# Kernel optimization log

Hardware: AMD Instinct MI355X
Metric: run time of the kernel (lower is better)

Reference implementation:

```python
import jax, jax.numpy as jnp
import numpy as np

S, B, D, H, F = 2048, 4, 1024, 16, 4096
DH = D // H  # per-head dim (nhid)
EPS = 1e-5


def layer_norm(x, g, b):
    m = jnp.mean(x, axis=-1, keepdims=True)
    v = jnp.mean((x - m) ** 2, axis=-1, keepdims=True)
    return (x - m) * jax.lax.rsqrt(v + EPS) * g + b


def setup_inputs() -> dict:
    key = jax.random.key(0)
    ks = jax.random.split(key, 16)
    s = 1.0 / np.sqrt(D)
    sf = 1.0 / np.sqrt(F)
    return {
        "x": jax.random.normal(ks[0], (S, B, D), dtype=jnp.float32),
        "ln1_g": jnp.ones((D,), jnp.float32),
        "ln1_b": jnp.zeros((D,), jnp.float32),
        "ln2_g": jnp.ones((D,), jnp.float32),
        "ln2_b": jnp.zeros((D,), jnp.float32),
        "Wq": jax.random.normal(ks[1], (D, D), jnp.float32) * s,
        "bq": jnp.zeros((D,), jnp.float32),
        "Wk": jax.random.normal(ks[2], (D, D), jnp.float32) * s,
        "bk": jnp.zeros((D,), jnp.float32),
        "Wv": jax.random.normal(ks[3], (D, D), jnp.float32) * s,
        "bv": jnp.zeros((D,), jnp.float32),
        "Wo": jax.random.normal(ks[4], (D, D), jnp.float32) * s,
        "bo": jnp.zeros((D,), jnp.float32),
        "W1": jax.random.normal(ks[5], (D, F), jnp.float32) * s,
        "b1": jnp.zeros((F,), jnp.float32),
        "W2": jax.random.normal(ks[6], (F, D), jnp.float32) * sf,
        "b2": jnp.zeros((D,), jnp.float32),
    }


def reference(x, ln1_g, ln1_b, ln2_g, ln2_b, Wq, bq, Wk, bk, Wv, bv, Wo, bo, W1, b1, W2, b2):
    # --- sublayer 0: LN -> full (non-causal) multi-head self-attention -> residual ---
    h = layer_norm(x, ln1_g, ln1_b)                      # [S,B,D]
    q = (h @ Wq + bq).reshape(S, B, H, DH)
    k = (h @ Wk + bk).reshape(S, B, H, DH)
    v = (h @ Wv + bv).reshape(S, B, H, DH)
    scale = 1.0 / jnp.sqrt(jnp.asarray(DH, x.dtype))
    scores = jnp.einsum("sbhd,tbhd->bhst", q, k) * scale  # [B,H,S,S]
    attn = jax.nn.softmax(scores, axis=-1)
    ctx = jnp.einsum("bhst,tbhd->sbhd", attn, v).reshape(S, B, D)
    x = x + (ctx @ Wo + bo)
    # --- sublayer 1: LN -> position-wise FFN -> residual ---
    h2 = layer_norm(x, ln2_g, ln2_b)
    ff = jax.nn.relu(h2 @ W1 + b1) @ W2 + b2
    return x + ff
```

## Files before the change

### kernel.cpp

```cpp
#include <hip/hip_runtime.h>
#include <hip/hip_bf16.h>
#include <stdint.h>

constexpr int S = 2048;
constexpr int B = 4;
constexpr int D = 1024;
constexpr int H = 16;
constexpr int F = 4096;
constexpr int DH = 64;
constexpr int N = S * B;

typedef __attribute__((ext_vector_type(8))) short  bf16x8;
typedef __attribute__((ext_vector_type(4))) float  floatx4;

__device__ __forceinline__ unsigned short f2bf(float f) {
    __hip_bfloat16 h = __float2bfloat16(f);
    return __builtin_bit_cast(unsigned short, h);
}
__device__ __forceinline__ uint32_t pack_bf2_fast(float a, float b) {
    uint32_t ua = __builtin_bit_cast(uint32_t, a) + 0x8000u;
    uint32_t ub = __builtin_bit_cast(uint32_t, b) + 0x8000u;
    return (ua >> 16) | (ub & 0xffff0000u);
}
__device__ __forceinline__ void glds16(const unsigned short* g, unsigned short* l) {
    __builtin_amdgcn_global_load_lds((__attribute__((address_space(1))) void*)(g),
                                     (__attribute__((address_space(3))) void*)(l),
                                     16, 0, 0);
}

__global__ __launch_bounds__(256) void convert_transpose(
    const float* __restrict__ src, unsigned short* __restrict__ dst, int K, int M) {
    __shared__ float tile[32][33];
    const int m0 = blockIdx.x * 32;
    const int k0 = blockIdx.y * 32;
    const int tx = threadIdx.x;
    const int ty = threadIdx.y;
    #pragma unroll
    for (int i = 0; i < 32; i += 8)
        tile[ty + i][tx] = src[(size_t)(k0 + ty + i) * M + m0 + tx];
    __syncthreads();
    #pragma unroll
    for (int i = 0; i < 32; i += 8)
        dst[(size_t)(m0 + ty + i) * K + k0 + tx] = f2bf(tile[tx][ty + i]);
}

__global__ __launch_bounds__(256) void transpose_v(
    const unsigned short* __restrict__ v, unsigned short* __restrict__ vt) {
    __shared__ unsigned short t[64][72];
    const int tid = threadIdx.x;
    const int s0 = blockIdx.x * 64;
    const int h  = blockIdx.y;
    const int b  = blockIdx.z;
    #pragma unroll
    for (int i = 0; i < 2; i++) {
        int c = i * 256 + tid;
        int row = c >> 3, off = (c & 7) * 8;
        *(uint4*)&t[row][off] =
            *(const uint4*)(v + ((size_t)(s0 + row) * B + b) * D + h * 64 + off);
    }
    __syncthreads();
    #pragma unroll
    for (int i = 0; i < 2; i++) {
        int c = i * 256 + tid;
        int dh = c >> 3, off = (c & 7) * 8;
        unsigned short tmp[8];
        #pragma unroll
        for (int j = 0; j < 8; j++) tmp[j] = t[off + j][dh];
        *(uint4*)(vt + ((size_t)((b * H + h) * 64 + dh)) * S + s0 + off) = *(uint4*)tmp;
    }
}

__global__ __launch_bounds__(256) void ln_kernel(
    const float* __restrict__ x, const float* __restrict__ g,
    const float* __restrict__ b, unsigned short* __restrict__ out) {
    const int row = blockIdx.x;
    const int tid = threadIdx.x;
    float4 v = ((const float4*)(x + (size_t)row * D))[tid];
    float s  = v.x + v.y + v.z + v.w;
    float ss = v.x * v.x + v.y * v.y + v.z * v.z + v.w * v.w;
    #pragma unroll
    for (int o = 32; o > 0; o >>= 1) {
        s  += __shfl_down(s,  o, 64);
        ss += __shfl_down(ss, o, 64);
    }
    __shared__ float red[8];
    __shared__ float mv[2];
    const int wv = tid >> 6, ln = tid & 63;
    if (ln == 0) { red[wv] = s; red[4 + wv] = ss; }
    __syncthreads();
    if (tid == 0) {
        float S2 = red[0] + red[1] + red[2] + red[3];
        float SS = red[4] + red[5] + red[6] + red[7];
        float mean = S2 * (1.0f / D);
        float var  = SS * (1.0f / D) - mean * mean;
        mv[0] = mean;
        mv[1] = rsqrtf(var + 1e-5f);
    }
    __syncthreads();
    const float mean = mv[0], inv = mv[1];
    float4 gv = ((const float4*)g)[tid];
    float4 bv = ((const float4*)b)[tid];
    ushort4 o4;
    o4.x = f2bf((v.x - mean) * inv * gv.x + bv.x);
    o4.y = f2bf((v.y - mean) * inv * gv.y + bv.y);
    o4.z = f2bf((v.z - mean) * inv * gv.z + bv.z);
    o4.w = f2bf((v.w - mean) * inv * gv.w + bv.w);
    ((ushort4*)(out + (size_t)row * D))[tid] = o4;
}

template <int RELU, int RESID, int OUT_BF16>
__global__ __launch_bounds__(256, 2) void gemm_bt(
    const unsigned short* __restrict__ A,
    const unsigned short* __restrict__ Bt,
    const float* __restrict__ bias,
    const float* __restrict__ resid,
    void* __restrict__ out,
    int M, int K) {
    __shared__ __align__(16) unsigned short As[128 * 32];
    __shared__ __align__(16) unsigned short Bs[128 * 32];

    const int tid  = threadIdx.x;
    const int lane = tid & 63;
    const int wave = tid >> 6;
    const int wr = (wave >> 1) * 64;
    const int wc = (wave & 1) * 64;
    const int n0 = blockIdx.y * 128;
    const int m0 = blockIdx.x * 128;
    const int quad = lane >> 4;
    const int r    = lane & 15;

    floatx4 acc[4][4] = {};

    const int l4 = lane >> 2;
    const int lc = lane & 3;
    const int seg0 = 2 * wave, seg1 = 2 * wave + 1;
    const int rowA0 = seg0 * 16 + l4;
    const int rowA1 = seg1 * 16 + l4;
    const int kch0 = ((lc ^ ((rowA0 >> 1) & 3)) * 8);
    const int kch1 = ((lc ^ ((rowA1 >> 1) & 3)) * 8);
    const unsigned short* gA0 = A  + (size_t)(n0 + rowA0) * K + kch0;
    const unsigned short* gA1 = A  + (size_t)(n0 + rowA1) * K + kch1;
    const unsigned short* gB0 = Bt + (size_t)(m0 + rowA0) * K + kch0;
    const unsigned short* gB1 = Bt + (size_t)(m0 + rowA1) * K + kch1;
    unsigned short* lA0 = As + seg0 * 512;
    unsigned short* lA1 = As + seg1 * 512;
    unsigned short* lB0 = Bs + seg0 * 512;
    unsigned short* lB1 = Bs + seg1 * 512;

    const int fc = (quad ^ ((r >> 1) & 3)) * 8;

    for (int k0 = 0; k0 < K; k0 += 32) {
        __syncthreads();
        glds16(gA0, lA0);
        glds16(gA1, lA1);
        glds16(gB0, lB0);
        glds16(gB1, lB1);
        gA0 += 32; gA1 += 32; gB0 += 32; gB1 += 32;
        __syncthreads();

        bf16x8 af[4], bfr[4];
        #pragma unroll
        for (int i = 0; i < 4; i++)
            af[i] = *(const bf16x8*)&As[(wr + i * 16 + r) * 32 + fc];
        #pragma unroll
        for (int j = 0; j < 4; j++)
            bfr[j] = *(const bf16x8*)&Bs[(wc + j * 16 + r) * 32 + fc];
        #pragma unroll
        for (int i = 0; i < 4; i++)
            #pragma unroll
            for (int j = 0; j < 4; j++)
                acc[i][j] = __builtin_amdgcn_mfma_f32_16x16x32_bf16(af[i], bfr[j], acc[i][j], 0, 0, 0);
    }

    #pragma unroll
    for (int i = 0; i < 4; i++) {
        #pragma unroll
        for (int j = 0; j < 4; j++) {
            const int row = n0 + wr + i * 16 + quad * 4;
            const int col = m0 + wc + j * 16 + r;
            const float bcol = bias[col];
            #pragma unroll
            for (int rr = 0; rr < 4; rr++) {
                float val = acc[i][j][rr] + bcol;
                if constexpr (RESID) val += resid[(size_t)(row + rr) * M + col];
                if constexpr (RELU)  val = fmaxf(val, 0.0f);
                if constexpr (OUT_BF16)
                    ((unsigned short*)out)[(size_t)(row + rr) * M + col] = f2bf(val);
                else
                    ((float*)out)[(size_t)(row + rr) * M + col] = val;
            }
        }
    }
}

__global__ __launch_bounds__(256, 2) void flash_attn(
    const unsigned short* __restrict__ q,
    const unsigned short* __restrict__ k,
    const unsigned short* __restrict__ vt,
    unsigned short* __restrict__ ctx) {
    constexpr int LQK = 72;
    constexpr int LV  = 136;
    constexpr int LP  = 136;
    constexpr float SCL = 0.18033688011112042f;

    __shared__ __align__(16) unsigned short Ks[128 * LQK];
    __shared__ __align__(16) unsigned short Vs[64 * LV];
    __shared__ __align__(16) unsigned short Ps[128 * LP];

    const int tid  = threadIdx.x;
    const int lane = tid & 63;
    const int wave = tid >> 6;
    const int quad = lane >> 4;
    const int r    = lane & 15;
    const int s0 = blockIdx.x * 128;
    const int h  = blockIdx.y;
    const int b  = blockIdx.z;

    const int wkr = (wave >> 1) * 64;
    const int wqc = (wave & 1) * 64;
    const int wq0 = wave * 32;

    unsigned short* Qs = Ps;
    #pragma unroll
    for (int i = 0; i < 4; i++) {
        int c = i * 256 + tid;
        int row = c >> 3, off = (c & 7) * 8;
        *(uint4*)&Qs[row * LQK + off] =
            *(const uint4*)(q + ((size_t)(s0 + row) * B + b) * D + h * 64 + off);
    }
    __syncthreads();
    bf16x8 qf[4][2];
    #pragma unroll
    for (int j = 0; j < 4; j++)
        #pragma unroll
        for (int kk = 0; kk < 2; kk++)
            qf[j][kk] = *(const bf16x8*)&Qs[(wqc + j * 16 + r) * LQK + kk * 32 + quad * 8];
    __syncthreads();

    const bf16x8 ones = {(short)0x3F80, (short)0x3F80, (short)0x3F80, (short)0x3F80,
                         (short)0x3F80, (short)0x3F80, (short)0x3F80, (short)0x3F80};

    uint4 kr[4], vr[4];
    const unsigned short* kbase  = k  + (size_t)b * D + h * 64;
    const unsigned short* vtbase = vt + (size_t)((b * H + h) * 64) * S;
    {
        #pragma unroll
        for (int i = 0; i < 4; i++) {
            int c = i * 256 + tid;
            int row = c >> 3, off = (c & 7) * 8;
            kr[i] = *(const uint4*)(kbase + (size_t)row * B * D + off);
        }
        #pragma unroll
        for (int i = 0; i < 4; i++) {
            int c = i * 256 + tid;
            int row = c >> 4, off = (c & 15) * 8;
            vr[i] = *(const uint4*)(vtbase + (size_t)row * S + off);
        }
    }

    floatx4 acc2[2][4] = {};
    floatx4 accD[2]    = {};

    for (int t = 0; t < S / 128; t++) {
        __syncthreads();
        #pragma unroll
        for (int i = 0; i < 4; i++) {
            int c = i * 256 + tid;
            int row = c >> 3, off = (c & 7) * 8;
            *(uint4*)&Ks[row * LQK + off] = kr[i];
        }
        #pragma unroll
        for (int i = 0; i < 4; i++) {
            int c = i * 256 + tid;
            int row = c >> 4, off = (c & 15) * 8;
            *(uint4*)&Vs[row * LV + off] = vr[i];
        }
        __syncthreads();

        if (t + 1 < S / 128) {
            const size_t tb = (size_t)(t + 1) * 128;
            #pragma unroll
            for (int i = 0; i < 4; i++) {
                int c = i * 256 + tid;
                int row = c >> 3, off = (c & 7) * 8;
                kr[i] = *(const uint4*)(kbase + (tb + row) * B * D + off);
            }
            #pragma unroll
            for (int i = 0; i < 4; i++) {
                int c = i * 256 + tid;
                int row = c >> 4, off = (c & 15) * 8;
                vr[i] = *(const uint4*)(vtbase + (size_t)row * S + tb + off);
            }
        }

        #pragma unroll
        for (int i = 0; i < 4; i++) {
            floatx4 sci[4] = {};
            #pragma unroll
            for (int kk = 0; kk < 2; kk++) {
                bf16x8 kf = *(const bf16x8*)&Ks[(wkr + i * 16 + r) * LQK + kk * 32 + quad * 8];
                #pragma unroll
                for (int j = 0; j < 4; j++)
                    sci[j] = __builtin_amdgcn_mfma_f32_16x16x32_bf16(kf, qf[j][kk], sci[j], 0, 0, 0);
            }
            #pragma unroll
            for (int j = 0; j < 4; j++) {
                float p0 = exp2f(sci[j][0] * SCL);
                float p1 = exp2f(sci[j][1] * SCL);
                float p2 = exp2f(sci[j][2] * SCL);
                float p3 = exp2f(sci[j][3] * SCL);
                uint2 w;
                w.x = pack_bf2_fast(p0, p1);
                w.y = pack_bf2_fast(p2, p3);
                *(uint2*)&Ps[(wqc + j * 16 + r) * LP + wkr + i * 16 + quad * 4] = w;
            }
        }
        __syncthreads();

        #pragma unroll
        for (int ks = 0; ks < 4; ks++) {
            bf16x8 a2[2], b2[4];
            #pragma unroll
            for (int i2 = 0; i2 < 2; i2++)
                a2[i2] = *(const bf16x8*)&Ps[(wq0 + i2 * 16 + r) * LP + ks * 32 + quad * 8];
            #pragma unroll
            for (int jn = 0; jn < 4; jn++)
                b2[jn] = *(const bf16x8*)&Vs[(jn * 16 + r) * LV + ks * 32 + quad * 8];
            #pragma unroll
            for (int i2 = 0; i2 < 2; i2++) {
                #pragma unroll
                for (int jn = 0; jn < 4; jn++)
                    acc2[i2][jn] = __builtin_amdgcn_mfma_f32_16x16x32_bf16(a2[i2], b2[jn], acc2[i2][jn], 0, 0, 0);
                accD[i2] = __builtin_amdgcn_mfma_f32_16x16x32_bf16(a2[i2], ones, accD[i2], 0, 0, 0);
            }
        }
    }

    float inv[2][4];
    #pragma unroll
    for (int i2 = 0; i2 < 2; i2++)
        #pragma unroll
        for (int rr = 0; rr < 4; rr++)
            inv[i2][rr] = 1.0f / accD[i2][rr];

    #pragma unroll
    for (int i2 = 0; i2 < 2; i2++) {
        #pragma unroll
        for (int jn = 0; jn < 4; jn++) {
            #pragma unroll
            for (int rr = 0; rr < 4; rr++) {
                const int qrow = wq0 + i2 * 16 + quad * 4 + rr;
                const int dh   = jn * 16 + r;
                const float val = acc2[i2][jn][rr] * inv[i2][rr];
                ctx[((size_t)(s0 + qrow) * B + b) * D + h * 64 + dh] = f2bf(val);
            }
        }
    }
}

extern "C" void kernel_launch(void* const* d_in, const int* in_sizes, int n_in,
                              void* d_out, int out_size, void* d_ws, size_t ws_size,
                              hipStream_t stream) {
    const float* x    = (const float*)d_in[0];
    const float* ln1g = (const float*)d_in[1];
    const float* ln1b = (const float*)d_in[2];
    const float* ln2g = (const float*)d_in[3];
    const float* ln2b = (const float*)d_in[4];
    const float* Wq   = (const float*)d_in[5];
    const float* bq   = (const float*)d_in[6];
    const float* Wk   = (const float*)d_in[7];
    const float* bk   = (const float*)d_in[8];
    const float* Wv   = (const float*)d_in[9];
    const float* bv   = (const float*)d_in[10];
    const float* Wo   = (const float*)d_in[11];
    const float* bo   = (const float*)d_in[12];
    const float* W1   = (const float*)d_in[13];
    const float* b1   = (const float*)d_in[14];
    const float* W2   = (const float*)d_in[15];
    const float* b2   = (const float*)d_in[16];
    float* out = (float*)d_out;

    char* ws = (char*)d_ws;
    const size_t MB = 1ull << 20;
    unsigned short* wqT = (unsigned short*)(ws + 0 * MB);
    unsigned short* wkT = (unsigned short*)(ws + 2 * MB);
    unsigned short* wvT = (unsigned short*)(ws + 4 * MB);
    unsigned short* woT = (unsigned short*)(ws + 6 * MB);
    unsigned short* w1T = (unsigned short*)(ws + 8 * MB);
    unsigned short* w2T = (unsigned short*)(ws + 16 * MB);
    unsigned short* h   = (unsigned short*)(ws + 24 * MB);
    unsigned short* qb  = (unsigned short*)(ws + 40 * MB);
    unsigned short* kb  = (unsigned short*)(ws + 56 * MB);
    unsigned short* vb  = (unsigned short*)(ws + 72 * MB);
    unsigned short* ctx = (unsigned short*)(ws + 88 * MB);
    float*          x1  = (float*)(ws + 104 * MB);
    unsigned short* vt  = (unsigned short*)(ws + 104 * MB);
    unsigned short* ff1 = qb;
    unsigned short* h2  = h;

    const dim3 tb(32, 8);
    convert_transpose<<<dim3(D / 32, D / 32), tb, 0, stream>>>(Wq, wqT, D, D);
    convert_transpose<<<dim3(D / 32, D / 32), tb, 0, stream>>>(Wk, wkT, D, D);
    convert_transpose<<<dim3(D / 32, D / 32), tb, 0, stream>>>(Wv, wvT, D, D);
    convert_transpose<<<dim3(D / 32, D / 32), tb, 0, stream>>>(Wo, woT, D, D);
    convert_transpose<<<dim3(F / 32, D / 32), tb, 0, stream>>>(W1, w1T, D, F);
    convert_transpose<<<dim3(D / 32, F / 32), tb, 0, stream>>>(W2, w2T, F, D);

    ln_kernel<<<N, 256, 0, stream>>>(x, ln1g, ln1b, h);

    const dim3 g1(D / 128, N / 128);
    gemm_bt<0, 0, 1><<<g1, 256, 0, stream>>>(h, wqT, bq, nullptr, qb, D, D);
    gemm_bt<0, 0, 1><<<g1, 256, 0, stream>>>(h, wkT, bk, nullptr, kb, D, D);
    gemm_bt<0, 0, 1><<<g1, 256, 0, stream>>>(h, wvT, bv, nullptr, vb, D, D);

    transpose_v<<<dim3(S / 64, H, B), 256, 0, stream>>>(vb, vt);

    flash_attn<<<dim3(S / 128, H, B), 256, 0, stream>>>(qb, kb, vt, ctx);

    gemm_bt<0, 1, 0><<<g1, 256, 0, stream>>>(ctx, woT, bo, x, x1, D, D);

    ln_kernel<<<N, 256, 0, stream>>>(x1, ln2g, ln2b, h2);

    gemm_bt<1, 0, 1><<<dim3(F / 128, N / 128), 256, 0, stream>>>(h2, w1T, b1, nullptr, ff1, F, D);

    gemm_bt<0, 1, 0><<<g1, 256, 0, stream>>>(ff1, w2T, b2, x1, out, D, F);
}
```

Baseline: 674.4 us.

## Make attention waves own their query rows and stream V from global

Each wave now computes the scores for its own 32 query rows against all 128 keys and writes only its own rows of P. That removes the barrier between the score and PV phases. V fragments are no longer staged in shared memory. They are loaded straight from global memory into registers, double-buffered across the four k-steps. With less shared memory, launch bounds rise to 3 blocks per SM for more occupancy. The trade-off is that each wave repeats K-fragment loads over all 128 keys, V global reads are duplicated across waves, and register pressure rises.

```diff
diff --git a/kernel.cpp b/kernel.cpp
--- a/kernel.cpp
+++ b/kernel.cpp
@@ -193,18 +193,16 @@
     }
 }
 
-__global__ __launch_bounds__(256, 2) void flash_attn(
+__global__ __launch_bounds__(256, 3) void flash_attn(
     const unsigned short* __restrict__ q,
     const unsigned short* __restrict__ k,
     const unsigned short* __restrict__ vt,
     unsigned short* __restrict__ ctx) {
     constexpr int LQK = 72;
-    constexpr int LV  = 136;
     constexpr int LP  = 136;
     constexpr float SCL = 0.18033688011112042f;
 
     __shared__ __align__(16) unsigned short Ks[128 * LQK];
-    __shared__ __align__(16) unsigned short Vs[64 * LV];
     __shared__ __align__(16) unsigned short Ps[128 * LP];
 
     const int tid  = threadIdx.x;
@@ -215,12 +213,9 @@
     const int s0 = blockIdx.x * 128;
     const int h  = blockIdx.y;
     const int b  = blockIdx.z;
-
-    const int wkr = (wave >> 1) * 64;
-    const int wqc = (wave & 1) * 64;
     const int wq0 = wave * 32;
 
-    unsigned short* Qs = Ps;
+    unsigned short* Qs = Ks;
     #pragma unroll
     for (int i = 0; i < 4; i++) {
         int c = i * 256 + tid;
@@ -229,33 +224,24 @@
             *(const uint4*)(q + ((size_t)(s0 + row) * B + b) * D + h * 64 + off);
     }
     __syncthreads();
-    bf16x8 qf[4][2];
-    #pragma unroll
-    for (int j = 0; j < 4; j++)
+    bf16x8 qf[2][2];
+    #pragma unroll
+    for (int j = 0; j < 2; j++)
         #pragma unroll
         for (int kk = 0; kk < 2; kk++)
-            qf[j][kk] = *(const bf16x8*)&Qs[(wqc + j * 16 + r) * LQK + kk * 32 + quad * 8];
-    __syncthreads();
+            qf[j][kk] = *(const bf16x8*)&Qs[(wq0 + j * 16 + r) * LQK + kk * 32 + quad * 8];
 
     const bf16x8 ones = {(short)0x3F80, (short)0x3F80, (short)0x3F80, (short)0x3F80,
                          (short)0x3F80, (short)0x3F80, (short)0x3F80, (short)0x3F80};
 
-    uint4 kr[4], vr[4];
+    uint4 kr[4];
     const unsigned short* kbase  = k  + (size_t)b * D + h * 64;
     const unsigned short* vtbase = vt + (size_t)((b * H + h) * 64) * S;
-    {
-        #pragma unroll
-        for (int i = 0; i < 4; i++) {
-            int c = i * 256 + tid;
-            int row = c >> 3, off = (c & 7) * 8;
-            kr[i] = *(const uint4*)(kbase + (size_t)row * B * D + off);
-        }
-        #pragma unroll
-        for (int i = 0; i < 4; i++) {
-            int c = i * 256 + tid;
-            int row = c >> 4, off = (c & 15) * 8;
-            vr[i] = *(const uint4*)(vtbase + (size_t)row * S + off);
-        }
+    #pragma unroll
+    for (int i = 0; i < 4; i++) {
+        int c = i * 256 + tid;
+        int row = c >> 3, off = (c & 7) * 8;
+        kr[i] = *(const uint4*)(kbase + (size_t)row * B * D + off);
     }
 
     floatx4 acc2[2][4] = {};
@@ -269,12 +255,6 @@
             int row = c >> 3, off = (c & 7) * 8;
             *(uint4*)&Ks[row * LQK + off] = kr[i];
         }
-        #pragma unroll
-        for (int i = 0; i < 4; i++) {
-            int c = i * 256 + tid;
-            int row = c >> 4, off = (c & 15) * 8;
-            *(uint4*)&Vs[row * LV + off] = vr[i];
-        }
         __syncthreads();
 
         if (t + 1 < S / 128) {
@@ -285,73 +265,77 @@
                 int row = c >> 3, off = (c & 7) * 8;
                 kr[i] = *(const uint4*)(kbase + (tb + row) * B * D + off);
             }
-            #pragma unroll
-            for (int i = 0; i < 4; i++) {
-                int c = i * 256 + tid;
-                int row = c >> 4, off = (c & 15) * 8;
-                vr[i] = *(const uint4*)(vtbase + (size_t)row * S + tb + off);
-            }
-        }
-
-        #pragma unroll
-        for (int i = 0; i < 4; i++) {
-            floatx4 sci[4] = {};
-            #pragma unroll
-            for (int kk = 0; kk < 2; kk++) {
-                bf16x8 kf = *(const bf16x8*)&Ks[(wkr + i * 16 + r) * LQK + kk * 32 + quad * 8];
-                #pragma unroll
-                for (int j = 0; j < 4; j++)
-                    sci[j] = __builtin_amdgcn_mfma_f32_16x16x32_bf16(kf, qf[j][kk], sci[j], 0, 0, 0);
-            }
-            #pragma unroll
-            for (int j = 0; j < 4; j++) {
-                float p0 = exp2f(sci[j][0] * SCL);
-                float p1 = exp2f(sci[j][1] * SCL);
-                float p2 = exp2f(sci[j][2] * SCL);
-                float p3 = exp2f(sci[j][3] * SCL);
+        }
+
+        const unsigned short* vrow = vtbase + (size_t)r * S + t * 128 + quad * 8;
+        uint4 vbuf[2][4];
+        #pragma unroll
+        for (int ss = 0; ss < 2; ss++)
+            #pragma unroll
+            for (int jn = 0; jn < 4; jn++)
+                vbuf[ss][jn] = *(const uint4*)(vrow + (size_t)(jn * 16) * S + ss * 32);
+
+        #pragma unroll
+        for (int i = 0; i < 8; i++) {
+            bf16x8 kf0 = *(const bf16x8*)&Ks[(i * 16 + r) * LQK + quad * 8];
+            bf16x8 kf1 = *(const bf16x8*)&Ks[(i * 16 + r) * LQK + 32 + quad * 8];
+            #pragma unroll
+            for (int j = 0; j < 2; j++) {
+                floatx4 sc = {};
+                sc = __builtin_amdgcn_mfma_f32_16x16x32_bf16(kf0, qf[j][0], sc, 0, 0, 0);
+                sc = __builtin_amdgcn_mfma_f32_16x16x32_bf16(kf1, qf[j][1], sc, 0, 0, 0);
+                float p0 = exp2f(sc[0] * SCL);
+                float p1 = exp2f(sc[1] * SCL);
+                float p2 = exp2f(sc[2] * SCL);
+                float p3 = exp2f(sc[3] * SCL);
                 uint2 w;
                 w.x = pack_bf2_fast(p0, p1);
                 w.y = pack_bf2_fast(p2, p3);
-                *(uint2*)&Ps[(wqc + j * 16 + r) * LP + wkr + i * 16 + quad * 4] = w;
-            }
-        }
-        __syncthreads();
-
-        #pragma unroll
-        for (int ks = 0; ks < 4; ks++) {
-            bf16x8 a2[2], b2[4];
-            #pragma unroll
-            for (int i2 = 0; i2 < 2; i2++)
-                a2[i2] = *(const bf16x8*)&Ps[(wq0 + i2 * 16 + r) * LP + ks * 32 + quad * 8];
+                *(uint2*)&Ps[(wq0 + j * 16 + r) * LP + i * 16 + quad * 4] = w;
+            }
+        }
+
+        #pragma unroll
+        for (int s = 0; s < 4; s++) {
+            bf16x8 a2[2];
+            #pragma unroll
+            for (int j = 0; j < 2; j++)
+                a2[j] = *(const bf16x8*)&Ps[(wq0 + j * 16 + r) * LP + s * 32 + quad * 8];
+            bf16x8 b2[4];
             #pragma unroll
             for (int jn = 0; jn < 4; jn++)
-                b2[jn] = *(const bf16x8*)&Vs[(jn * 16 + r) * LV + ks * 32 + quad * 8];
-            #pragma unroll
-            for (int i2 = 0; i2 < 2; i2++) {
+                b2[jn] = __builtin_bit_cast(bf16x8, vbuf[s & 1][jn]);
+            if (s < 2) {
                 #pragma unroll
                 for (int jn = 0; jn < 4; jn++)
-                    acc2[i2][jn] = __builtin_amdgcn_mfma_f32_16x16x32_bf16(a2[i2], b2[jn], acc2[i2][jn], 0, 0, 0);
-                accD[i2] = __builtin_amdgcn_mfma_f32_16x16x32_bf16(a2[i2], ones, accD[i2], 0, 0, 0);
+                    vbuf[s & 1][jn] = *(const uint4*)(vrow + (size_t)(jn * 16) * S + (s + 2) * 32);
+            }
+            #pragma unroll
+            for (int j = 0; j < 2; j++) {
+                #pragma unroll
+                for (int jn = 0; jn < 4; jn++)
+                    acc2[j][jn] = __builtin_amdgcn_mfma_f32_16x16x32_bf16(a2[j], b2[jn], acc2[j][jn], 0, 0, 0);
+                accD[j] = __builtin_amdgcn_mfma_f32_16x16x32_bf16(a2[j], ones, accD[j], 0, 0, 0);
             }
         }
     }
 
     float inv[2][4];
     #pragma unroll
-    for (int i2 = 0; i2 < 2; i2++)
+    for (int j = 0; j < 2; j++)
         #pragma unroll
         for (int rr = 0; rr < 4; rr++)
-            inv[i2][rr] = 1.0f / accD[i2][rr];
-
-    #pragma unroll
-    for (int i2 = 0; i2 < 2; i2++) {
+            inv[j][rr] = 1.0f / accD[j][rr];
+
+    #pragma unroll
+    for (int j = 0; j < 2; j++) {
         #pragma unroll
         for (int jn = 0; jn < 4; jn++) {
             #pragma unroll
             for (int rr = 0; rr < 4; rr++) {
-                const int qrow = wq0 + i2 * 16 + quad * 4 + rr;
+                const int qrow = wq0 + j * 16 + quad * 4 + rr;
                 const int dh   = jn * 16 + r;
-                const float val = acc2[i2][jn][rr] * inv[i2][rr];
+                const float val = acc2[j][jn][rr] * inv[j][rr];
                 ctx[((size_t)(s0 + qrow) * B + b) * D + h * 64 + dh] = f2bf(val);
             }
         }
```

Measured after the change: 666.6 us. About the same (-1.2%).
